# Optimization experiments

Hardware: AMD Instinct MI355X
Metric: run time of the kernel (lower is better)

## Reference

```python
import jax, jax.numpy as jnp
import numpy as np

N = 1024      # total ROIs packed across the ragged batch
S = 14        # roi_output_size
C = 256       # conv_dim == feature_size
NC = 80       # num_classes
K = 4         # num_convs
DN = ('NHWC', 'HWIO', 'NHWC')


def setup_inputs() -> dict:
    key = jax.random.key(0)
    ks = jax.random.split(key, 5)
    x = jax.random.normal(ks[0], (N, S, S, C), jnp.float32)
    # 4 identical-shape 3x3 convs (C->C), stacked on a leading axis
    Wc = jax.random.normal(ks[1], (K, 3, 3, C, C), jnp.float32) * 0.03
    bc = jnp.zeros((K, C), jnp.float32)
    # 2x2 stride-2 transpose conv (C->C)
    Wt = jax.random.normal(ks[2], (2, 2, C, C), jnp.float32) * 0.03
    bt = jnp.zeros((C,), jnp.float32)
    # 1x1 mask predictor (C->NC), no activation
    Wm = jax.random.normal(ks[3], (1, 1, C, NC), jnp.float32) * 0.03
    bm = jnp.zeros((NC,), jnp.float32)
    return {"x": x, "Wc": Wc, "bc": bc, "Wt": Wt, "bt": bt, "Wm": Wm, "bm": bm}


def reference(x, Wc, bc, Wt, bt, Wm, bm):
    # Packed-batch equivalent of the nested tf.map_fn: conv math is
    # independent per ROI, so one batched conv over all ROIs is identical.
    for i in range(K):  # fixed small layer count
        x = jax.lax.conv_general_dilated(x, Wc[i], (1, 1), 'SAME', dimension_numbers=DN)
        x = jax.nn.relu(x + bc[i])
    # Conv2DTranspose(kernel=2, stride=2, padding='valid'), relu
    x = jax.lax.conv_transpose(x, Wt, (2, 2), 'VALID', dimension_numbers=DN)
    x = jax.nn.relu(x + bt)
    # 1x1 conv, linear activation -> [N, 28, 28, NC]
    x = jax.lax.conv_general_dilated(x, Wm, (1, 1), 'SAME', dimension_numbers=DN) + bm
    return x
```

## Files before the change

kernel.cpp:

```cpp
#include <hip/hip_runtime.h>


typedef _Float16 f16x8 __attribute__((ext_vector_type(8)));
typedef float    f32x4 __attribute__((ext_vector_type(4)));
typedef unsigned short u16;
typedef unsigned int   u32;

__device__ __forceinline__ u16 f2h(float f) {
  union { _Float16 h; u16 u; } c; c.h = (_Float16)f; return c.u;
}

__device__ __forceinline__ void store8(u16* dst, const u16* o) {
  uint4 v;
  v.x = (u32)o[0] | ((u32)o[1] << 16);
  v.y = (u32)o[2] | ((u32)o[3] << 16);
  v.z = (u32)o[4] | ((u32)o[5] << 16);
  v.w = (u32)o[6] | ((u32)o[7] << 16);
  *(uint4*)dst = v;
}

__global__ void prep_weights(const float* __restrict__ Wc, const float* __restrict__ Wt,
                             const float* __restrict__ Wm,
                             u16* __restrict__ WbP, u16* __restrict__ WtP,
                             u16* __restrict__ WmP) {
  int id = blockIdx.x * 256 + threadIdx.x;
  u16 o[8];
  if (id < 294912) {
    int li = id & 63; int rest = id >> 6;
    int ct = rest & 15; rest >>= 4;
    int kc = rest & 7;  rest >>= 3;
    int co  = ct * 16 + (li & 15);
    int ci0 = kc * 32 + (li >> 4) * 8;
#pragma unroll
    for (int j = 0; j < 8; j++) o[j] = f2h(Wc[(rest * 256 + ci0 + j) * 256 + co]);
    store8(&WbP[id * 8], o);
  } else if (id < 327680) {
    int id2 = id - 294912;
    int li = id2 & 63; int rest = id2 >> 6;
    int ct = rest & 15; rest >>= 4;
    int kc = rest & 7;  rest >>= 3;
    int srcq = 3 - rest;
    int co  = ct * 16 + (li & 15);
    int ci0 = kc * 32 + (li >> 4) * 8;
#pragma unroll
    for (int j = 0; j < 8; j++) o[j] = f2h(Wt[(srcq * 256 + ci0 + j) * 256 + co]);
    store8(&WtP[id2 * 8], o);
  } else if (id < 330240) {
    int id3 = id - 327680;
    int li = id3 & 63; int rest = id3 >> 6;
    int kc = rest / 5, nt = rest % 5;
    int nc  = nt * 16 + (li & 15);
    int ci0 = kc * 32 + (li >> 4) * 8;
#pragma unroll
    for (int j = 0; j < 8; j++) o[j] = f2h(Wm[(ci0 + j) * 80 + nc]);
    store8(&WmP[id3 * 8], o);
  }
}

template <bool INF32>
__global__ __launch_bounds__(256, 2)
void conv_layer(const void* __restrict__ in_, const u16* __restrict__ WbP,
                const float* __restrict__ bc, u16* __restrict__ out, int layer) {
  __shared__ u16 sA[196 * 136 + 128];
  const int ZP = 196 * 136;
  const int tid = threadIdx.x;
  const int w = tid >> 6, lane = tid & 63, q = lane >> 4, r = lane & 15;
  const int roi = blockIdx.x, mbase = blockIdx.y * 112;
  if (tid < 64) ((u32*)(sA + ZP))[tid] = 0u;

  int py[7], px[7];
#pragma unroll
  for (int mt = 0; mt < 7; mt++) {
    int p = mbase + mt * 16 + r;
    py[mt] = (p < 196) ? (p / 14) : 1000;
    px[mt] = p % 14;
  }
  f32x4 acc[7][4];
#pragma unroll
  for (int mt = 0; mt < 7; mt++)
#pragma unroll
    for (int nf = 0; nf < 4; nf++) acc[mt][nf] = (f32x4){0.f, 0.f, 0.f, 0.f};

  const float* xin = (const float*)in_;
  const u16*   yin = (const u16*)in_;

  for (int kh = 0; kh < 2; kh++) {
    if (kh) __syncthreads();
    if (INF32) {
      for (int c = tid; c < 196 * 32; c += 256) {
        int pix = c >> 5, c4 = (c & 31) * 4;
        const float4 v = *(const float4*)&xin[(roi * 196 + pix) * 256 + kh * 128 + c4];
        ushort4 h; h.x = f2h(v.x); h.y = f2h(v.y); h.z = f2h(v.z); h.w = f2h(v.w);
        *(ushort4*)&sA[pix * 136 + c4] = h;
      }
    } else {
      for (int c = tid; c < 196 * 16; c += 256) {
        int pix = c >> 4, c8 = (c & 15) * 8;
        *(uint4*)&sA[pix * 136 + c8] =
            *(const uint4*)&yin[(roi * 196 + pix) * 256 + kh * 128 + c8];
      }
    }
    __syncthreads();

    for (int tap = 0; tap < 9; tap++) {
      const int dy = tap / 3 - 1, dx = tap % 3 - 1;
      int offs[7];
#pragma unroll
      for (int mt = 0; mt < 7; mt++) {
        int ny = py[mt] + dy, nx = px[mt] + dx;
        bool v = ((u32)ny < 14u) && ((u32)nx < 14u);
        offs[mt] = v ? (ny * 14 + nx) * 136 : ZP;
      }
#pragma unroll
      for (int kk = 0; kk < 4; kk++) {
        const int kc = kh * 4 + kk;
        f16x8 b[4];
#pragma unroll
        for (int nf = 0; nf < 4; nf++)
          b[nf] = *(const f16x8*)&WbP[((((layer * 9 + tap) * 8 + kc) * 16 + (w * 4 + nf)) * 64 + lane) * 8];
#pragma unroll
        for (int mt = 0; mt < 7; mt++) {
          f16x8 a = *(const f16x8*)&sA[offs[mt] + kk * 32 + q * 8];
#pragma unroll
          for (int nf = 0; nf < 4; nf++)
            acc[mt][nf] = __builtin_amdgcn_mfma_f32_16x16x32_f16(a, b[nf], acc[mt][nf], 0, 0, 0);
        }
      }
    }
  }

  float bias[4];
#pragma unroll
  for (int nf = 0; nf < 4; nf++) bias[nf] = bc[layer * 256 + (w * 4 + nf) * 16 + r];
#pragma unroll
  for (int mt = 0; mt < 7; mt++) {
#pragma unroll
    for (int jj = 0; jj < 4; jj++) {
      int p = mbase + mt * 16 + q * 4 + jj;
      if (p < 196) {
#pragma unroll
        for (int nf = 0; nf < 4; nf++) {
          float v = acc[mt][nf][jj] + bias[nf];
          v = fmaxf(v, 0.f);
          out[(roi * 196 + p) * 256 + (w * 4 + nf) * 16 + r] = f2h(v);
        }
      }
    }
  }
}

__global__ __launch_bounds__(256, 2)
void tail_fused(const u16* __restrict__ y4, const u16* __restrict__ WtP,
                const u16* __restrict__ WmP, const float* __restrict__ bt,
                const float* __restrict__ bm, float* __restrict__ out) {
  __shared__ u16 sA[112 * 264 + 128];
  const int ZP = 112 * 264;
  const int tid = threadIdx.x;
  const int w = tid >> 6, lane = tid & 63, q = lane >> 4, r = lane & 15;
  const int roi = blockIdx.x, ab = blockIdx.y, mbase = blockIdx.z * 112;
  if (tid < 64) ((u32*)(sA + ZP))[tid] = 0u;

  int offs[7];
#pragma unroll
  for (int mt = 0; mt < 7; mt++) {
    int p = mbase + mt * 16 + r;
    offs[mt] = (p < 196) ? p * 136 : ZP;
  }
  f32x4 acc[7][4];
#pragma unroll
  for (int mt = 0; mt < 7; mt++)
#pragma unroll
    for (int nf = 0; nf < 4; nf++) acc[mt][nf] = (f32x4){0.f, 0.f, 0.f, 0.f};

  for (int kh = 0; kh < 2; kh++) {
    if (kh) __syncthreads();
    for (int c = tid; c < 196 * 16; c += 256) {
      int pix = c >> 4, c8 = (c & 15) * 8;
      *(uint4*)&sA[pix * 136 + c8] =
          *(const uint4*)&y4[(roi * 196 + pix) * 256 + kh * 128 + c8];
    }
    __syncthreads();
#pragma unroll
    for (int kk = 0; kk < 4; kk++) {
      const int kc = kh * 4 + kk;
      f16x8 b[4];
#pragma unroll
      for (int nf = 0; nf < 4; nf++)
        b[nf] = *(const f16x8*)&WtP[(((ab * 8 + kc) * 16 + (w * 4 + nf)) * 64 + lane) * 8];
#pragma unroll
      for (int mt = 0; mt < 7; mt++) {
        f16x8 a = *(const f16x8*)&sA[offs[mt] + kk * 32 + q * 8];
#pragma unroll
        for (int nf = 0; nf < 4; nf++)
          acc[mt][nf] = __builtin_amdgcn_mfma_f32_16x16x32_f16(a, b[nf], acc[mt][nf], 0, 0, 0);
      }
    }
  }

  __syncthreads();
  float btv[4];
#pragma unroll
  for (int nf = 0; nf < 4; nf++) btv[nf] = bt[(w * 4 + nf) * 16 + r];
#pragma unroll
  for (int mt = 0; mt < 7; mt++) {
#pragma unroll
    for (int jj = 0; jj < 4; jj++) {
      int row = mt * 16 + q * 4 + jj;
#pragma unroll
      for (int nf = 0; nf < 4; nf++) {
        float v = fmaxf(acc[mt][nf][jj] + btv[nf], 0.f);
        sA[row * 264 + (w * 4 + nf) * 16 + r] = f2h(v);
      }
    }
  }
  __syncthreads();

  float bmv[5];
#pragma unroll
  for (int nt = 0; nt < 5; nt++) bmv[nt] = bm[nt * 16 + r];
  const int a_ = ab >> 1, b_ = ab & 1;
  for (int tt = w; tt < 7; tt += 4) {
    f32x4 a2[5];
#pragma unroll
    for (int nt = 0; nt < 5; nt++) a2[nt] = (f32x4){0.f, 0.f, 0.f, 0.f};
#pragma unroll
    for (int kc = 0; kc < 8; kc++) {
      f16x8 af = *(const f16x8*)&sA[(tt * 16 + r) * 264 + kc * 32 + q * 8];
#pragma unroll
      for (int nt = 0; nt < 5; nt++) {
        f16x8 bw = *(const f16x8*)&WmP[((kc * 5 + nt) * 64 + lane) * 8];
        a2[nt] = __builtin_amdgcn_mfma_f32_16x16x32_f16(af, bw, a2[nt], 0, 0, 0);
      }
    }
#pragma unroll
    for (int jj = 0; jj < 4; jj++) {
      int row = tt * 16 + q * 4 + jj;
      int p = mbase + row;
      if (p < 196) {
        int y = p / 14, x = p % 14;
        int base = roi * 62720 + (2 * y + a_) * 2240 + (2 * x + b_) * 80;
#pragma unroll
        for (int nt = 0; nt < 5; nt++) out[base + nt * 16 + r] = a2[nt][jj] + bmv[nt];
      }
    }
  }
}

extern "C" void kernel_launch(void* const* d_in, const int* in_sizes, int n_in,
                              void* d_out, int out_size, void* d_ws, size_t ws_size,
                              hipStream_t stream) {
  const float* x  = (const float*)d_in[0];
  const float* Wc = (const float*)d_in[1];
  const float* bc = (const float*)d_in[2];
  const float* Wt = (const float*)d_in[3];
  const float* bt = (const float*)d_in[4];
  const float* Wm = (const float*)d_in[5];
  const float* bm = (const float*)d_in[6];
  float* out = (float*)d_out;

  char* ws = (char*)d_ws;
  u16* WbP = (u16*)(ws);
  u16* WtP = (u16*)(ws + 4718592);
  u16* WmP = (u16*)(ws + 5242880);
  u16* yA  = (u16*)(ws + 6291456);
  u16* yB  = (u16*)(ws + 6291456 + 102760448);

  prep_weights<<<1290, 256, 0, stream>>>(Wc, Wt, Wm, WbP, WtP, WmP);

  dim3 cg(1024, 2);
  conv_layer<true ><<<cg, 256, 0, stream>>>(x,  WbP, bc, yA, 0);
  conv_layer<false><<<cg, 256, 0, stream>>>(yA, WbP, bc, yB, 1);
  conv_layer<false><<<cg, 256, 0, stream>>>(yB, WbP, bc, yA, 2);
  conv_layer<false><<<cg, 256, 0, stream>>>(yA, WbP, bc, yB, 3);

  tail_fused<<<dim3(1024, 4, 2), 256, 0, stream>>>(yB, WtP, WmP, bt, bm, out);
}
```

Baseline: 1.671 ms.

## Retile conv into 64-pixel halo blocks with swizzled LDS and prefetched weights

Each conv block now covers 64 output pixels instead of 112 and loads a 96-pixel halo window with all 256 channels in one pass, replacing the two half-channel passes. Shared-memory rows are XOR-swizzled to avoid bank conflicts. Weight fragments are double-buffered across K steps, and occupancy rises to 3 blocks per CU. The tail kernel loads its input tile once and loops over the four transpose-conv sub-positions inside the block, removing redundant input loads. The cost is more halo re-reads across blocks and more blocks, each doing less work.

```diff
diff --git a/kernel.cpp b/kernel.cpp
--- a/kernel.cpp
+++ b/kernel.cpp
@@ -58,91 +58,121 @@
 }
 
 template <bool INF32>
-__global__ __launch_bounds__(256, 2)
+__global__ __launch_bounds__(256, 3)
 void conv_layer(const void* __restrict__ in_, const u16* __restrict__ WbP,
                 const float* __restrict__ bc, u16* __restrict__ out, int layer) {
-  __shared__ u16 sA[196 * 136 + 128];
-  const int ZP = 196 * 136;
+  __shared__ u16 sA[97 * 256];
   const int tid = threadIdx.x;
   const int w = tid >> 6, lane = tid & 63, q = lane >> 4, r = lane & 15;
-  const int roi = blockIdx.x, mbase = blockIdx.y * 112;
-  if (tid < 64) ((u32*)(sA + ZP))[tid] = 0u;
-
-  int py[7], px[7];
-#pragma unroll
-  for (int mt = 0; mt < 7; mt++) {
-    int p = mbase + mt * 16 + r;
-    py[mt] = (p < 196) ? (p / 14) : 1000;
-    px[mt] = p % 14;
-  }
-  f32x4 acc[7][4];
-#pragma unroll
-  for (int mt = 0; mt < 7; mt++)
+  const int roi = blockIdx.x, P0 = blockIdx.y * 64;
+  const int pixbase = P0 - 15;
+
+  if (tid < 128) ((u32*)(sA + 96 * 256))[tid] = 0u;
+
+  if (INF32) {
+    const float* xin = (const float*)in_;
+    for (int i = tid; i < 3072; i += 256) {
+      int lp = i >> 5, c = i & 31;
+      int g = pixbase + lp;
+      uint4 d = {0u, 0u, 0u, 0u};
+      if ((u32)g < 196u) {
+        const float* s = &xin[((roi * 196 + g) << 8) + c * 8];
+        float4 v0 = *(const float4*)s;
+        float4 v1 = *(const float4*)(s + 4);
+        d.x = (u32)f2h(v0.x) | ((u32)f2h(v0.y) << 16);
+        d.y = (u32)f2h(v0.z) | ((u32)f2h(v0.w) << 16);
+        d.z = (u32)f2h(v1.x) | ((u32)f2h(v1.y) << 16);
+        d.w = (u32)f2h(v1.z) | ((u32)f2h(v1.w) << 16);
+      }
+      *(uint4*)((char*)sA + lp * 512 + ((c ^ (lp & 7)) << 4)) = d;
+    }
+  } else {
+    const u16* yin = (const u16*)in_;
+    for (int i = tid; i < 3072; i += 256) {
+      int lp = i >> 5, c = i & 31;
+      int g = pixbase + lp;
+      uint4 d = {0u, 0u, 0u, 0u};
+      if ((u32)g < 196u) d = *(const uint4*)&yin[((roi * 196 + g) << 8) + c * 8];
+      *(uint4*)((char*)sA + lp * 512 + ((c ^ (lp & 7)) << 4)) = d;
+    }
+  }
+
+  int py[4], px[4], lpb[4];
+#pragma unroll
+  for (int mt = 0; mt < 4; mt++) {
+    int p = P0 + mt * 16 + r;
+    py[mt] = p / 14; px[mt] = p % 14;
+    lpb[mt] = mt * 16 + r + 15;
+  }
+  f32x4 acc[4][4];
+#pragma unroll
+  for (int mt = 0; mt < 4; mt++)
 #pragma unroll
     for (int nf = 0; nf < 4; nf++) acc[mt][nf] = (f32x4){0.f, 0.f, 0.f, 0.f};
 
-  const float* xin = (const float*)in_;
-  const u16*   yin = (const u16*)in_;
-
-  for (int kh = 0; kh < 2; kh++) {
-    if (kh) __syncthreads();
-    if (INF32) {
-      for (int c = tid; c < 196 * 32; c += 256) {
-        int pix = c >> 5, c4 = (c & 31) * 4;
-        const float4 v = *(const float4*)&xin[(roi * 196 + pix) * 256 + kh * 128 + c4];
-        ushort4 h; h.x = f2h(v.x); h.y = f2h(v.y); h.z = f2h(v.z); h.w = f2h(v.w);
-        *(ushort4*)&sA[pix * 136 + c4] = h;
-      }
-    } else {
-      for (int c = tid; c < 196 * 16; c += 256) {
-        int pix = c >> 4, c8 = (c & 15) * 8;
-        *(uint4*)&sA[pix * 136 + c8] =
-            *(const uint4*)&yin[(roi * 196 + pix) * 256 + kh * 128 + c8];
-      }
-    }
-    __syncthreads();
-
-    for (int tap = 0; tap < 9; tap++) {
-      const int dy = tap / 3 - 1, dx = tap % 3 - 1;
-      int offs[7];
-#pragma unroll
-      for (int mt = 0; mt < 7; mt++) {
-        int ny = py[mt] + dy, nx = px[mt] + dx;
-        bool v = ((u32)ny < 14u) && ((u32)nx < 14u);
-        offs[mt] = v ? (ny * 14 + nx) * 136 : ZP;
-      }
-#pragma unroll
-      for (int kk = 0; kk < 4; kk++) {
-        const int kc = kh * 4 + kk;
-        f16x8 b[4];
-#pragma unroll
-        for (int nf = 0; nf < 4; nf++)
-          b[nf] = *(const f16x8*)&WbP[((((layer * 9 + tap) * 8 + kc) * 16 + (w * 4 + nf)) * 64 + lane) * 8];
-#pragma unroll
-        for (int mt = 0; mt < 7; mt++) {
-          f16x8 a = *(const f16x8*)&sA[offs[mt] + kk * 32 + q * 8];
-#pragma unroll
-          for (int nf = 0; nf < 4; nf++)
-            acc[mt][nf] = __builtin_amdgcn_mfma_f32_16x16x32_f16(a, b[nf], acc[mt][nf], 0, 0, 0);
-        }
-      }
-    }
+  __syncthreads();
+
+  const u16* Bp = WbP + (size_t)layer * 589824;
+  const u32 q16 = (u32)(q << 4);
+  u32 base[4], key[4];
+
+  auto setoffs = [&](int t) {
+    int tap = t >> 3;
+    int dy = tap / 3 - 1, dx = tap % 3 - 1;
+    int d = dy * 14 + dx;
+#pragma unroll
+    for (int mt = 0; mt < 4; mt++) {
+      int ny = py[mt] + dy, nx = px[mt] + dx;
+      bool v = ((u32)ny < 14u) && ((u32)nx < 14u);
+      int lp = lpb[mt] + d;
+      base[mt] = v ? (u32)(lp * 512) : (u32)(96 * 512);
+      key[mt]  = v ? (u32)((lp & 7) << 4) : 0u;
+    }
+  };
+  auto loadb = [&](f16x8* b, int t) {
+#pragma unroll
+    for (int nf = 0; nf < 4; nf++)
+      b[nf] = *(const f16x8*)&Bp[(t * 16 + w * 4 + nf) * 512 + lane * 8];
+  };
+  auto step = [&](int t, const f16x8* b) {
+    int kk = t & 7;
+    u32 kq = (u32)(kk << 6) | q16;
+    f16x8 a[4];
+#pragma unroll
+    for (int mt = 0; mt < 4; mt++)
+      a[mt] = *(const f16x8*)((const char*)sA + (base[mt] + (kq ^ key[mt])));
+#pragma unroll
+    for (int mt = 0; mt < 4; mt++)
+#pragma unroll
+      for (int nf = 0; nf < 4; nf++)
+        acc[mt][nf] = __builtin_amdgcn_mfma_f32_16x16x32_f16(a[mt], b[nf], acc[mt][nf], 0, 0, 0);
+  };
+
+  f16x8 bcur[4], bnxt[4];
+  setoffs(0);
+  loadb(bcur, 0);
+#pragma unroll 4
+  for (int t = 0; t < 72; t += 2) {
+    loadb(bnxt, t + 1);
+    step(t, bcur);
+    loadb(bcur, (t + 2 < 72) ? (t + 2) : 71);
+    step(t + 1, bnxt);
+    if (((t + 2) & 7) == 0 && (t + 2) < 72) setoffs(t + 2);
   }
 
   float bias[4];
 #pragma unroll
   for (int nf = 0; nf < 4; nf++) bias[nf] = bc[layer * 256 + (w * 4 + nf) * 16 + r];
 #pragma unroll
-  for (int mt = 0; mt < 7; mt++) {
+  for (int mt = 0; mt < 4; mt++) {
 #pragma unroll
     for (int jj = 0; jj < 4; jj++) {
-      int p = mbase + mt * 16 + q * 4 + jj;
+      int p = P0 + mt * 16 + q * 4 + jj;
       if (p < 196) {
 #pragma unroll
         for (int nf = 0; nf < 4; nf++) {
-          float v = acc[mt][nf][jj] + bias[nf];
-          v = fmaxf(v, 0.f);
-          out[(roi * 196 + p) * 256 + (w * 4 + nf) * 16 + r] = f2h(v);
+          float v = fmaxf(acc[mt][nf][jj] + bias[nf], 0.f);
+          out[((roi * 196 + p) << 8) + (w * 4 + nf) * 16 + r] = f2h(v);
         }
       }
     }
@@ -153,94 +183,96 @@
 void tail_fused(const u16* __restrict__ y4, const u16* __restrict__ WtP,
                 const u16* __restrict__ WmP, const float* __restrict__ bt,
                 const float* __restrict__ bm, float* __restrict__ out) {
-  __shared__ u16 sA[112 * 264 + 128];
-  const int ZP = 112 * 264;
+  __shared__ u16 sIn[64 * 256];
+  __shared__ u16 sT[64 * 256];
   const int tid = threadIdx.x;
   const int w = tid >> 6, lane = tid & 63, q = lane >> 4, r = lane & 15;
-  const int roi = blockIdx.x, ab = blockIdx.y, mbase = blockIdx.z * 112;
-  if (tid < 64) ((u32*)(sA + ZP))[tid] = 0u;
-
-  int offs[7];
-#pragma unroll
-  for (int mt = 0; mt < 7; mt++) {
-    int p = mbase + mt * 16 + r;
-    offs[mt] = (p < 196) ? p * 136 : ZP;
-  }
-  f32x4 acc[7][4];
-#pragma unroll
-  for (int mt = 0; mt < 7; mt++)
-#pragma unroll
-    for (int nf = 0; nf < 4; nf++) acc[mt][nf] = (f32x4){0.f, 0.f, 0.f, 0.f};
-
-  for (int kh = 0; kh < 2; kh++) {
-    if (kh) __syncthreads();
-    for (int c = tid; c < 196 * 16; c += 256) {
-      int pix = c >> 4, c8 = (c & 15) * 8;
-      *(uint4*)&sA[pix * 136 + c8] =
-          *(const uint4*)&y4[(roi * 196 + pix) * 256 + kh * 128 + c8];
-    }
-    __syncthreads();
-#pragma unroll
-    for (int kk = 0; kk < 4; kk++) {
-      const int kc = kh * 4 + kk;
+  const int roi = blockIdx.x, P0 = blockIdx.y * 64;
+
+  for (int i = tid; i < 2048; i += 256) {
+    int lp = i >> 5, c = i & 31;
+    int g = P0 + lp;
+    uint4 d = {0u, 0u, 0u, 0u};
+    if (g < 196) d = *(const uint4*)&y4[((roi * 196 + g) << 8) + c * 8];
+    *(uint4*)((char*)sIn + lp * 512 + ((c ^ (lp & 7)) << 4)) = d;
+  }
+  __syncthreads();
+
+  float btv[4];
+#pragma unroll
+  for (int nf = 0; nf < 4; nf++) btv[nf] = bt[(w * 4 + nf) * 16 + r];
+  float bmv[5];
+#pragma unroll
+  for (int nt = 0; nt < 5; nt++) bmv[nt] = bm[nt * 16 + r];
+  const u32 q16 = (u32)(q << 4);
+
+  for (int ab = 0; ab < 4; ab++) {
+    f32x4 acc[4][4];
+#pragma unroll
+    for (int mt = 0; mt < 4; mt++)
+#pragma unroll
+      for (int nf = 0; nf < 4; nf++) acc[mt][nf] = (f32x4){0.f, 0.f, 0.f, 0.f};
+
+#pragma unroll
+    for (int kk = 0; kk < 8; kk++) {
       f16x8 b[4];
 #pragma unroll
       for (int nf = 0; nf < 4; nf++)
-        b[nf] = *(const f16x8*)&WtP[(((ab * 8 + kc) * 16 + (w * 4 + nf)) * 64 + lane) * 8];
-#pragma unroll
-      for (int mt = 0; mt < 7; mt++) {
-        f16x8 a = *(const f16x8*)&sA[offs[mt] + kk * 32 + q * 8];
+        b[nf] = *(const f16x8*)&WtP[((ab * 8 + kk) * 16 + w * 4 + nf) * 512 + lane * 8];
+      u32 kq = (u32)(kk << 6) | q16;
+#pragma unroll
+      for (int mt = 0; mt < 4; mt++) {
+        int lp = mt * 16 + r;
+        f16x8 a = *(const f16x8*)((const char*)sIn + lp * 512 + ((kq ^ (u32)((lp & 7) << 4))));
 #pragma unroll
         for (int nf = 0; nf < 4; nf++)
           acc[mt][nf] = __builtin_amdgcn_mfma_f32_16x16x32_f16(a, b[nf], acc[mt][nf], 0, 0, 0);
       }
     }
-  }
-
-  __syncthreads();
-  float btv[4];
-#pragma unroll
-  for (int nf = 0; nf < 4; nf++) btv[nf] = bt[(w * 4 + nf) * 16 + r];
-#pragma unroll
-  for (int mt = 0; mt < 7; mt++) {
+
+    if (ab) __syncthreads();
+#pragma unroll
+    for (int mt = 0; mt < 4; mt++) {
+#pragma unroll
+      for (int jj = 0; jj < 4; jj++) {
+        int row = mt * 16 + q * 4 + jj;
+#pragma unroll
+        for (int nf = 0; nf < 4; nf++) {
+          int ch = (w * 4 + nf) * 16 + r;
+          int c = ch >> 3, e = ch & 7;
+          float v = fmaxf(acc[mt][nf][jj] + btv[nf], 0.f);
+          *(u16*)((char*)sT + row * 512 + ((c ^ (row & 7)) << 4) + e * 2) = f2h(v);
+        }
+      }
+    }
+    __syncthreads();
+
+    f32x4 a2[5];
+#pragma unroll
+    for (int nt = 0; nt < 5; nt++) a2[nt] = (f32x4){0.f, 0.f, 0.f, 0.f};
+    {
+      int lp = w * 16 + r;
+      u32 rowbase = (u32)(lp * 512), rkey = (u32)((lp & 7) << 4);
+#pragma unroll
+      for (int kk = 0; kk < 8; kk++) {
+        u32 kq = (u32)(kk << 6) | q16;
+        f16x8 af = *(const f16x8*)((const char*)sT + rowbase + (kq ^ rkey));
+#pragma unroll
+        for (int nt = 0; nt < 5; nt++) {
+          f16x8 bw = *(const f16x8*)&WmP[((kk * 5 + nt) * 64 + lane) * 8];
+          a2[nt] = __builtin_amdgcn_mfma_f32_16x16x32_f16(af, bw, a2[nt], 0, 0, 0);
+        }
+      }
+    }
+    const int a_ = ab >> 1, b_ = ab & 1;
 #pragma unroll
     for (int jj = 0; jj < 4; jj++) {
-      int row = mt * 16 + q * 4 + jj;
-#pragma unroll
-      for (int nf = 0; nf < 4; nf++) {
-        float v = fmaxf(acc[mt][nf][jj] + btv[nf], 0.f);
-        sA[row * 264 + (w * 4 + nf) * 16 + r] = f2h(v);
-      }
-    }
-  }
-  __syncthreads();
-
-  float bmv[5];
-#pragma unroll
-  for (int nt = 0; nt < 5; nt++) bmv[nt] = bm[nt * 16 + r];
-  const int a_ = ab >> 1, b_ = ab & 1;
-  for (int tt = w; tt < 7; tt += 4) {
-    f32x4 a2[5];
-#pragma unroll
-    for (int nt = 0; nt < 5; nt++) a2[nt] = (f32x4){0.f, 0.f, 0.f, 0.f};
-#pragma unroll
-    for (int kc = 0; kc < 8; kc++) {
-      f16x8 af = *(const f16x8*)&sA[(tt * 16 + r) * 264 + kc * 32 + q * 8];
-#pragma unroll
-      for (int nt = 0; nt < 5; nt++) {
-        f16x8 bw = *(const f16x8*)&WmP[((kc * 5 + nt) * 64 + lane) * 8];
-        a2[nt] = __builtin_amdgcn_mfma_f32_16x16x32_f16(af, bw, a2[nt], 0, 0, 0);
-      }
-    }
-#pragma unroll
-    for (int jj = 0; jj < 4; jj++) {
-      int row = tt * 16 + q * 4 + jj;
-      int p = mbase + row;
+      int p = P0 + w * 16 + q * 4 + jj;
       if (p < 196) {
         int y = p / 14, x = p % 14;
-        int base = roi * 62720 + (2 * y + a_) * 2240 + (2 * x + b_) * 80;
-#pragma unroll
-        for (int nt = 0; nt < 5; nt++) out[base + nt * 16 + r] = a2[nt][jj] + bmv[nt];
+        int obase = roi * 62720 + (2 * y + a_) * 2240 + (2 * x + b_) * 80;
+#pragma unroll
+        for (int nt = 0; nt < 5; nt++) out[obase + nt * 16 + r] = a2[nt][jj] + bmv[nt];
       }
     }
   }
@@ -267,11 +299,11 @@
 
   prep_weights<<<1290, 256, 0, stream>>>(Wc, Wt, Wm, WbP, WtP, WmP);
 
-  dim3 cg(1024, 2);
+  dim3 cg(1024, 4);
   conv_layer<true ><<<cg, 256, 0, stream>>>(x,  WbP, bc, yA, 0);
   conv_layer<false><<<cg, 256, 0, stream>>>(yA, WbP, bc, yB, 1);
   conv_layer<false><<<cg, 256, 0, stream>>>(yB, WbP, bc, yA, 2);
   conv_layer<false><<<cg, 256, 0, stream>>>(yA, WbP, bc, yB, 3);
 
-  tail_fused<<<dim3(1024, 4, 2), 256, 0, stream>>>(yB, WtP, WmP, bt, bm, out);
-}
+  tail_fused<<<dim3(1024, 4), 256, 0, stream>>>(yB, WtP, WmP, bt, bm, out);
+}
```

After: 2.106 ms. 26.0% more time.
